# Kernel tuning notes

Measured on AMD Instinct MI355X. Metric: run time of the kernel, lower is better.

The kernel has to match this reference:

```python
import jax, jax.numpy as jnp
import numpy as np

MARGIN = 0.35
EPS = 1e-12  # matches F.normalize default eps


def setup_inputs() -> dict:
    key = jax.random.key(0)
    k1, k2 = jax.random.split(key)
    B, N, D = 64, 1024, 128
    embeddings = jax.random.normal(k1, (B, N, D), dtype=jnp.float32)
    labels = jax.random.randint(k2, (B, N), 0, 2, dtype=jnp.int64)
    return {"embeddings": embeddings, "labels": labels}


def reference(embeddings, labels):
    # L2-normalize along last dim (F.normalize semantics)
    norm = jnp.linalg.norm(embeddings, axis=-1, keepdims=True)
    emb = embeddings / jnp.maximum(norm, EPS)  # [B, N, D]

    pos = (labels == 1)  # [B, N]
    neg = (labels == 0)  # [B, N]
    n_pos = pos.sum(axis=-1)  # [B]
    n_neg = neg.sum(axis=-1)  # [B]
    valid = (n_pos > 0) & (n_neg > 0)  # [B]

    # pairwise similarity: positive i vs negative j within each sample
    sim = jnp.einsum('bnd,bmd->bnm', emb, emb)  # [B, N, N]
    hinge = jax.nn.relu(sim - 0.5 + MARGIN)  # [B, N, N]

    # per-positive mean over negatives
    neg_f = neg.astype(emb.dtype)
    per_pos_sum = jnp.einsum('bnm,bm->bn', hinge, neg_f)  # sum over negatives
    denom = jnp.maximum(n_neg, 1).astype(emb.dtype)[:, None]
    per_pos_mean = per_pos_sum / denom  # [B, N]

    pos_f = pos.astype(emb.dtype)
    valid_f = valid.astype(emb.dtype)
    loss_sum = jnp.sum(per_pos_mean * pos_f * valid_f[:, None])
    count = jnp.sum(n_pos * valid)
    return loss_sum / jnp.maximum(count, 1).astype(emb.dtype)
```

## Files before the change

kernel.cpp:

```cpp
#include <hip/hip_runtime.h>
#include <stdint.h>


#define B_    64
#define N_    1024
#define D_    128
#define NPAD  640
#define T_    5
#define NTILE (T_ * T_)

typedef __attribute__((ext_vector_type(4))) float floatx4;

__global__ __launch_bounds__(256) void scan_kernel(
    const long long* __restrict__ lab,
    unsigned short* __restrict__ posIdx,
    unsigned short* __restrict__ negIdx,
    int* __restrict__ npos)
{
    __shared__ int wsum[4];
    const int b = blockIdx.x, t = threadIdx.x;
    const int w = t >> 6, lane = t & 63;
    const long long* lb = lab + (size_t)b * N_;

    int l[4], c = 0;
    #pragma unroll
    for (int i = 0; i < 4; ++i) { l[i] = (int)lb[t * 4 + i]; c += l[i]; }

    int sc = c;
    #pragma unroll
    for (int off = 1; off < 64; off <<= 1) {
        int v = __shfl_up(sc, off);
        if (lane >= off) sc += v;
    }
    if (lane == 63) wsum[w] = sc;
    __syncthreads();
    int base = 0;
    for (int k = 0; k < w; ++k) base += wsum[k];

    int pe = base + sc - c;
    #pragma unroll
    for (int i = 0; i < 4; ++i) {
        const int n = t * 4 + i;
        if (l[i]) { if (pe < NPAD) posIdx[b * NPAD + pe] = (unsigned short)n; }
        else      { const int ne = n - pe; if (ne < NPAD) negIdx[b * NPAD + ne] = (unsigned short)n; }
        pe += l[i];
    }
    if (t == 255) npos[b] = base + sc;
}

__global__ __launch_bounds__(256) void prep_kernel(
    const float* __restrict__ emb,
    const unsigned short* __restrict__ posIdx,
    const unsigned short* __restrict__ negIdx,
    const int* __restrict__ npos,
    unsigned int* __restrict__ Apos_c,
    unsigned int* __restrict__ Aneg_c)
{
    const int w    = threadIdx.x >> 6;
    const int lane = threadIdx.x & 63;
    const int gw   = blockIdx.x * 4 + w;
    const int half = lane >> 5, sl = lane & 31;

    const int side = gw >= (B_ * NPAD / 2);
    const int p2   = side ? gw - (B_ * NPAD / 2) : gw;
    const int b    = p2 / (NPAD / 2);
    const int slot = (p2 % (NPAD / 2)) * 2 + half;

    const int np    = npos[b];
    const int count = side ? (N_ - np) : np;
    const unsigned short* idxArr = side ? negIdx : posIdx;

    float4 v = make_float4(0.f, 0.f, 0.f, 0.f);
    if (slot < count) {
        const int n = idxArr[b * NPAD + slot];
        v = *(const float4*)(emb + ((size_t)(b * N_ + n)) * D_ + sl * 4);
    }
    float ss = v.x * v.x + v.y * v.y + v.z * v.z + v.w * v.w;
    #pragma unroll
    for (int off = 16; off; off >>= 1) ss += __shfl_xor(ss, off);
    const float scale = 1.0f / fmaxf(sqrtf(ss), 1e-12f);

    unsigned int pk = 0;
    pk = __builtin_amdgcn_cvt_pk_fp8_f32(v.x * scale, v.y * scale, pk, false);
    pk = __builtin_amdgcn_cvt_pk_fp8_f32(v.z * scale, v.w * scale, pk, true);

    unsigned int* dst = side ? Aneg_c : Apos_c;
    dst[(size_t)(b * NPAD + slot) * (D_ / 4) + sl] = pk;
}

__global__ __launch_bounds__(256, 3) void gemm_hinge_kernel(
    const unsigned char* __restrict__ Apos_c,
    const unsigned char* __restrict__ Aneg_c,
    const int* __restrict__ npos,
    float* __restrict__ Stile)
{
    __shared__ unsigned char ldsA[128 * 128];
    __shared__ unsigned char ldsB[128 * 128];
    __shared__ float sred[4];

    const int t    = threadIdx.x;
    const int w    = t >> 6;
    const int lane = t & 63;
    const int tm = blockIdx.x, tn = blockIdx.y, b = blockIdx.z;

    const int np = npos[b];
    const int nn = N_ - np;
    const bool active = (tm * 128 < np) && (tn * 128 < nn);

    float tileSum = 0.f;
    if (active) {
        const char* gA = (const char*)(Apos_c + ((size_t)b * NPAD + (size_t)tm * 128) * D_);
        const char* gB = (const char*)(Aneg_c + ((size_t)b * NPAD + (size_t)tn * 128) * D_);
        auto lA = (__attribute__((address_space(3))) char*)ldsA;
        auto lB = (__attribute__((address_space(3))) char*)ldsB;

        #pragma unroll
        for (int it = 0; it < 4; ++it) {
            const int p   = it * 4096 + t * 16;
            const int row = p >> 7;
            const int c   = (p >> 4) & 7;
            const int goff = (row << 7) | ((c ^ (row & 7)) << 4);
            __builtin_amdgcn_global_load_lds(
                (const __attribute__((address_space(1))) void*)(gA + goff),
                (__attribute__((address_space(3))) void*)(lA + it * 4096 + w * 1024),
                16, 0, 0);
            __builtin_amdgcn_global_load_lds(
                (const __attribute__((address_space(1))) void*)(gB + goff),
                (__attribute__((address_space(3))) void*)(lB + it * 4096 + w * 1024),
                16, 0, 0);
        }
        __syncthreads();

        const int wm = w & 1, wn = w >> 1;
        const int r = lane & 15, quad = lane >> 4;
        const int rx = r & 7;

        floatx4 acc[4][4] = {};
        #pragma unroll
        for (int ks = 0; ks < 4; ++ks) {
            long af[4], bf[4];
            const int boff = (((ks * 2 + (quad >> 1)) ^ rx) << 4) + (quad & 1) * 8;
            #pragma unroll
            for (int i = 0; i < 4; ++i) {
                af[i] = *(const long*)(ldsA + (wm * 64 + i * 16 + r) * 128 + boff);
                bf[i] = *(const long*)(ldsB + (wn * 64 + i * 16 + r) * 128 + boff);
            }
            #pragma unroll
            for (int i = 0; i < 4; ++i)
                #pragma unroll
                for (int j = 0; j < 4; ++j)
                    acc[i][j] = __builtin_amdgcn_mfma_f32_16x16x32_fp8_fp8(
                        af[i], bf[j], acc[i][j], 0, 0, 0);
        }

        float s = 0.f;
        #pragma unroll
        for (int i = 0; i < 4; ++i)
            #pragma unroll
            for (int j = 0; j < 4; ++j)
                #pragma unroll
                for (int k2 = 0; k2 < 4; ++k2)
                    s += fmaxf(acc[i][j][k2] - 0.15f, 0.f);

        #pragma unroll
        for (int off = 32; off; off >>= 1) s += __shfl_down(s, off);
        if (lane == 0) sred[w] = s;
        __syncthreads();
        tileSum = sred[0] + sred[1] + sred[2] + sred[3];
    }

    if (t == 0) Stile[b * NTILE + tm * T_ + tn] = tileSum;
}

__global__ void finalize_kernel(const float* __restrict__ Stile,
                                const int* __restrict__ npos,
                                float* __restrict__ out)
{
    const int b = threadIdx.x;
    const int np = npos[b];
    const int nn = N_ - np;
    float S = 0.f;
    #pragma unroll
    for (int k = 0; k < NTILE; ++k) S += Stile[b * NTILE + k];
    const bool valid = (np > 0) && (nn > 0);
    float ls = valid ? S / (float)nn : 0.f;
    float c  = valid ? (float)np : 0.f;
    #pragma unroll
    for (int off = 32; off; off >>= 1) {
        ls += __shfl_down(ls, off);
        c  += __shfl_down(c, off);
    }
    if (b == 0) out[0] = ls / fmaxf(c, 1.f);
}

extern "C" void kernel_launch(void* const* d_in, const int* in_sizes, int n_in,
                              void* d_out, int out_size, void* d_ws, size_t ws_size,
                              hipStream_t stream)
{
    const float*     emb = (const float*)d_in[0];
    const long long* lab = (const long long*)d_in[1];
    float* out = (float*)d_out;

    char* ws = (char*)d_ws;
    float* Stile = (float*)ws;
    int*   npos  = (int*)(ws + (16 << 10));
    unsigned short* posIdx = (unsigned short*)(ws + (32 << 10));
    unsigned short* negIdx = (unsigned short*)(ws + (160 << 10));
    unsigned int* Apos_c = (unsigned int*)(ws + (1 << 20));
    unsigned int* Aneg_c = Apos_c + (size_t)B_ * NPAD * (D_ / 4);

    scan_kernel<<<B_, 256, 0, stream>>>(lab, posIdx, negIdx, npos);

    prep_kernel<<<B_ * NPAD / 4, 256, 0, stream>>>(
        emb, posIdx, negIdx, npos, Apos_c, Aneg_c);

    dim3 grid(T_, T_, B_);
    gemm_hinge_kernel<<<grid, 256, 0, stream>>>(
        (const unsigned char*)Apos_c, (const unsigned char*)Aneg_c, npos, Stile);

    finalize_kernel<<<1, 64, 0, stream>>>(Stile, npos, out);
}
```

Baseline: 92.09 us.

## Fuse label scan into embedding prep kernel using per-block LDS compaction

```diff
diff --git a/kernel.cpp b/kernel.cpp
--- a/kernel.cpp
+++ b/kernel.cpp
@@ -8,25 +8,27 @@
 #define NPAD  640
 #define T_    5
 #define NTILE (T_ * T_)
+#define PBLK  8
+#define SLOTS_PER_BLK (2 * NPAD / PBLK)
 
 typedef __attribute__((ext_vector_type(4))) float floatx4;
 
-__global__ __launch_bounds__(256) void scan_kernel(
+__global__ __launch_bounds__(1024) void prepscan_kernel(
+    const float* __restrict__ emb,
     const long long* __restrict__ lab,
-    unsigned short* __restrict__ posIdx,
-    unsigned short* __restrict__ negIdx,
+    unsigned int* __restrict__ Apos_c,
+    unsigned int* __restrict__ Aneg_c,
     int* __restrict__ npos)
 {
-    __shared__ int wsum[4];
-    const int b = blockIdx.x, t = threadIdx.x;
-    const int w = t >> 6, lane = t & 63;
-    const long long* lb = lab + (size_t)b * N_;
-
-    int l[4], c = 0;
-    #pragma unroll
-    for (int i = 0; i < 4; ++i) { l[i] = (int)lb[t * 4 + i]; c += l[i]; }
-
-    int sc = c;
+    __shared__ int wsum[16];
+    __shared__ unsigned short posLds[NPAD];
+    __shared__ unsigned short negLds[NPAD];
+
+    const int t = threadIdx.x, w = t >> 6, lane = t & 63;
+    const int b = blockIdx.y;
+
+    const int l = (int)lab[(size_t)b * N_ + t];
+    int sc = l;
     #pragma unroll
     for (int off = 1; off < 64; off <<= 1) {
         int v = __shfl_up(sc, off);
@@ -34,58 +36,45 @@
     }
     if (lane == 63) wsum[w] = sc;
     __syncthreads();
-    int base = 0;
-    for (int k = 0; k < w; ++k) base += wsum[k];
-
-    int pe = base + sc - c;
-    #pragma unroll
-    for (int i = 0; i < 4; ++i) {
-        const int n = t * 4 + i;
-        if (l[i]) { if (pe < NPAD) posIdx[b * NPAD + pe] = (unsigned short)n; }
-        else      { const int ne = n - pe; if (ne < NPAD) negIdx[b * NPAD + ne] = (unsigned short)n; }
-        pe += l[i];
-    }
-    if (t == 255) npos[b] = base + sc;
-}
-
-__global__ __launch_bounds__(256) void prep_kernel(
-    const float* __restrict__ emb,
-    const unsigned short* __restrict__ posIdx,
-    const unsigned short* __restrict__ negIdx,
-    const int* __restrict__ npos,
-    unsigned int* __restrict__ Apos_c,
-    unsigned int* __restrict__ Aneg_c)
-{
-    const int w    = threadIdx.x >> 6;
-    const int lane = threadIdx.x & 63;
-    const int gw   = blockIdx.x * 4 + w;
+    int base = 0, tot = 0;
+    #pragma unroll
+    for (int k = 0; k < 16; ++k) {
+        const int v = wsum[k];
+        tot += v;
+        if (k < w) base += v;
+    }
+    const int ep = base + sc - l;
+    if (l) { if (ep < NPAD) posLds[ep] = (unsigned short)t; }
+    else   { const int ne = t - ep; if (ne < NPAD) negLds[ne] = (unsigned short)t; }
+    const int np = tot;
+    if (blockIdx.x == 0 && t == 0) npos[b] = np;
+    __syncthreads();
+
     const int half = lane >> 5, sl = lane & 31;
-
-    const int side = gw >= (B_ * NPAD / 2);
-    const int p2   = side ? gw - (B_ * NPAD / 2) : gw;
-    const int b    = p2 / (NPAD / 2);
-    const int slot = (p2 % (NPAD / 2)) * 2 + half;
-
-    const int np    = npos[b];
-    const int count = side ? (N_ - np) : np;
-    const unsigned short* idxArr = side ? negIdx : posIdx;
-
-    float4 v = make_float4(0.f, 0.f, 0.f, 0.f);
-    if (slot < count) {
-        const int n = idxArr[b * NPAD + slot];
-        v = *(const float4*)(emb + ((size_t)(b * N_ + n)) * D_ + sl * 4);
-    }
-    float ss = v.x * v.x + v.y * v.y + v.z * v.z + v.w * v.w;
-    #pragma unroll
-    for (int off = 16; off; off >>= 1) ss += __shfl_xor(ss, off);
-    const float scale = 1.0f / fmaxf(sqrtf(ss), 1e-12f);
-
-    unsigned int pk = 0;
-    pk = __builtin_amdgcn_cvt_pk_fp8_f32(v.x * scale, v.y * scale, pk, false);
-    pk = __builtin_amdgcn_cvt_pk_fp8_f32(v.z * scale, v.w * scale, pk, true);
-
-    unsigned int* dst = side ? Aneg_c : Apos_c;
-    dst[(size_t)(b * NPAD + slot) * (D_ / 4) + sl] = pk;
+    #pragma unroll
+    for (int it = 0; it < 5; ++it) {
+        const int g    = blockIdx.x * SLOTS_PER_BLK + it * 32 + ((w << 1) | half);
+        const int side = (g >= NPAD);
+        const int slot = g - (side ? NPAD : 0);
+        const int count = side ? (N_ - np) : np;
+
+        float4 v = make_float4(0.f, 0.f, 0.f, 0.f);
+        if (slot < count) {
+            const int n = side ? negLds[slot] : posLds[slot];
+            v = *(const float4*)(emb + ((size_t)(b * N_ + n)) * D_ + sl * 4);
+        }
+        float ss = v.x * v.x + v.y * v.y + v.z * v.z + v.w * v.w;
+        #pragma unroll
+        for (int off = 16; off; off >>= 1) ss += __shfl_xor(ss, off);
+        const float scale = 1.0f / fmaxf(sqrtf(ss), 1e-12f);
+
+        unsigned int pk = 0;
+        pk = __builtin_amdgcn_cvt_pk_fp8_f32(v.x * scale, v.y * scale, pk, false);
+        pk = __builtin_amdgcn_cvt_pk_fp8_f32(v.z * scale, v.w * scale, pk, true);
+
+        unsigned int* dst = side ? Aneg_c : Apos_c;
+        dst[(size_t)(b * NPAD + slot) * (D_ / 4) + sl] = pk;
+    }
 }
 
 __global__ __launch_bounds__(256, 3) void gemm_hinge_kernel(
@@ -204,15 +193,11 @@
     char* ws = (char*)d_ws;
     float* Stile = (float*)ws;
     int*   npos  = (int*)(ws + (16 << 10));
-    unsigned short* posIdx = (unsigned short*)(ws + (32 << 10));
-    unsigned short* negIdx = (unsigned short*)(ws + (160 << 10));
     unsigned int* Apos_c = (unsigned int*)(ws + (1 << 20));
     unsigned int* Aneg_c = Apos_c + (size_t)B_ * NPAD * (D_ / 4);
 
-    scan_kernel<<<B_, 256, 0, stream>>>(lab, posIdx, negIdx, npos);
-
-    prep_kernel<<<B_ * NPAD / 4, 256, 0, stream>>>(
-        emb, posIdx, negIdx, npos, Apos_c, Aneg_c);
+    dim3 pgrid(PBLK, B_);
+    prepscan_kernel<<<pgrid, 1024, 0, stream>>>(emb, lab, Apos_c, Aneg_c, npos);
 
     dim3 grid(T_, T_, B_);
     gemm_hinge_kernel<<<grid, 256, 0, stream>>>(
```

Result: faster. 90.11 us (-2.2%).
